# Performance work log

Hardware: AMD Instinct MI355X
Metric: run time of the kernel (lower is better)

The kernel has to match this reference:

```python
import jax, jax.numpy as jnp
import numpy as np

B, L, DIM, H = 2, 2048, 2048, 16
D = DIM // H
EPS = 1e-6
CAP = 50.0
SCALE = D ** -0.5


def _rms_norm(x, w):
    # x: [B,H,L,D], normalize over last dim
    scale = jax.lax.rsqrt(jnp.maximum(jnp.mean(x * x, axis=-1, keepdims=True), EPS))
    return w * x * scale


def _rotate_half(x):
    x1, x2 = jnp.split(x, 2, axis=-1)
    return jnp.concatenate([-x2, x1], axis=-1)


def setup_inputs() -> dict:
    key = jax.random.key(0)
    ks = jax.random.split(key, 6)
    x = jax.random.normal(ks[0], (B, L, DIM), dtype=jnp.float32)
    w_qkv = jax.random.normal(ks[1], (3 * DIM, DIM), dtype=jnp.float32) * (DIM ** -0.5)
    w_out = jax.random.normal(ks[2], (DIM, DIM), dtype=jnp.float32) * (DIM ** -0.5)
    q_norm_w = jnp.ones((D,), dtype=jnp.float32)
    k_norm_w = jnp.ones((D,), dtype=jnp.float32)
    # rope tables [L, D]
    inv_freq = 1.0 / (10000.0 ** (np.arange(0, D, 2, dtype=np.float32) / D))
    t = np.arange(L, dtype=np.float32)
    freqs = np.outer(t, inv_freq)  # [L, D/2]
    emb = np.concatenate([freqs, freqs], axis=-1)  # [L, D]
    cos = jnp.asarray(np.cos(emb), dtype=jnp.float32)
    sin = jnp.asarray(np.sin(emb), dtype=jnp.float32)
    # additive causal mask [1,1,L,L]
    causal = np.triu(np.full((L, L), -1e9, dtype=np.float32), k=1)
    mask = jnp.asarray(causal)[None, None]
    return {"x": x, "w_qkv": w_qkv, "w_out": w_out, "q_norm_w": q_norm_w,
            "k_norm_w": k_norm_w, "cos": cos, "sin": sin, "mask": mask}


def reference(x, w_qkv, w_out, q_norm_w, k_norm_w, cos, sin, mask):
    b, l, _ = x.shape
    qkv = jnp.einsum('bld,ed->ble', x, w_qkv).reshape(b, l, 3, H, D)
    q, k, v = [jnp.transpose(qkv[:, :, i], (0, 2, 1, 3)) for i in range(3)]  # [B,H,L,D]
    q = _rms_norm(q, q_norm_w)
    k = _rms_norm(k, k_norm_w)
    # rope: cos/sin are [L,D] -> [1,1,L,D]
    c = cos[-l:, :][None, None]
    s = sin[-l:, :][None, None]
    q = q * c + _rotate_half(q) * s
    k = k * c + _rotate_half(k) * s
    attn = jnp.einsum('bhqd,bhkd->bhqk', q, k) * SCALE
    attn = jnp.tanh(attn / CAP) * CAP + mask
    probs = jax.nn.softmax(attn, axis=-1)
    o = jnp.einsum('bhqk,bhkd->bhqd', probs, v)
    o = jnp.transpose(o, (0, 2, 1, 3)).reshape(b, l, H * D)
    out = jnp.einsum('bld,ed->ble', o, w_out)
    return (out, (k, v))
```

## Files before the change

kernel.cpp:

```cpp
#include <hip/hip_runtime.h>
#include <hip/hip_bf16.h>
#include <stdint.h>

#define LL 2048
#define DD 128
#define HH 16

typedef float f32x4 __attribute__((ext_vector_type(4)));
typedef float f32x16 __attribute__((ext_vector_type(16)));
typedef float f32x2 __attribute__((ext_vector_type(2)));
typedef short bf16x8 __attribute__((ext_vector_type(8)));
typedef short short4v __attribute__((ext_vector_type(4)));
typedef int int4v __attribute__((ext_vector_type(4)));
typedef float float4v __attribute__((ext_vector_type(4)));

__device__ __forceinline__ float bf2f(short s) {
  union { unsigned u; float f; } v; v.u = ((unsigned)(unsigned short)s) << 16; return v.f;
}
__device__ __forceinline__ short f2bf(float f) {
  union { float f; unsigned u; } v; v.f = f;
  unsigned u = v.u;
  u += 0x7fffu + ((u >> 16) & 1u);
  return (short)(u >> 16);
}
__device__ __forceinline__ unsigned cvtpk(float lo, float hi) {
  unsigned r;
  asm("v_cvt_pk_bf16_f32 %0, %1, %2" : "=v"(r) : "v"(lo), "v"(hi));
  return r;
}

__device__ __forceinline__ void gload_lds16(const void* g, void* lds) {
  __builtin_amdgcn_global_load_lds(
      (__attribute__((address_space(1))) unsigned int*)(void*)(uintptr_t)g,
      (__attribute__((address_space(3))) unsigned int*)lds, 16, 0, 0);
}

__global__ __launch_bounds__(256) void cast_all_kernel(
    const float* __restrict__ x, const float* __restrict__ wqkv,
    const float* __restrict__ wout, short* __restrict__ dst)
{
  long i4 = ((long)blockIdx.x * 256 + threadIdx.x) * 4;
  const float* src; long off;
  if (i4 < 8388608L)        { src = x;    off = i4; }
  else if (i4 < 20971520L)  { src = wqkv; off = i4 - 8388608L; }
  else                      { src = wout; off = i4 - 20971520L; }
  float4v v = *(const float4v*)(src + off);
  short4v o;
  o.x = f2bf(v.x); o.y = f2bf(v.y); o.z = f2bf(v.z); o.w = f2bf(v.w);
  *(short4v*)(dst + i4) = o;
}

#define SCHED __builtin_amdgcn_sched_barrier(0)
#define BARRIER { __builtin_amdgcn_s_barrier(); }

#define STAGE(buf, opx, ptr, rb, ks, t)                                        \
  { _Pragma("unroll") for (int l_ = 0; l_ < 2; ++l_) {                          \
      int ch_ = l_ * 512 + tid;                                                 \
      int row_ = ch_ >> 2, ci_ = ch_ & 3;                                       \
      gload_lds16(ptr + (size_t)(rb + row_) * K + (t) * 64 + (ks) * 32 +        \
                      ((ci_ ^ ((row_ >> 1) & 3)) << 3),                         \
                  &lds[buf][opx][ks][ch_ << 3]);                                \
  } }

#define LDA(buf, mh, ks)                                                       \
  { _Pragma("unroll") for (int mf_ = 0; mf_ < 4; ++mf_) {                       \
      int r_ = wm * 128 + (mh) * 64 + mf_ * 16 + j;                             \
      areg[mf_] = *(const bf16x8*)&lds[buf][0][ks][r_ * 32 + ((g ^ ((j >> 1) & 3)) << 3)]; \
  } }

#define LDB(dst, buf, ks)                                                      \
  { _Pragma("unroll") for (int nf_ = 0; nf_ < 4; ++nf_) {                       \
      int r_ = wn * 64 + nf_ * 16 + j;                                          \
      dst[nf_] = *(const bf16x8*)&lds[buf][1][ks][r_ * 32 + ((g ^ ((j >> 1) & 3)) << 3)]; \
  } }

#define MFMAQ(mh, breg)                                                        \
  { __builtin_amdgcn_s_setprio(1);                                             \
    _Pragma("unroll") for (int mf_ = 0; mf_ < 4; ++mf_)                         \
      _Pragma("unroll") for (int nf_ = 0; nf_ < 4; ++nf_)                       \
        acc[(mh) * 4 + mf_][nf_] = __builtin_amdgcn_mfma_f32_16x16x32_bf16(     \
            areg[mf_], breg[nf_], acc[(mh) * 4 + mf_][nf_], 0, 0, 0);           \
    __builtin_amdgcn_s_setprio(0); }

__global__ __launch_bounds__(512, 2) void gemm256_kernel(
    const short* __restrict__ A, const short* __restrict__ Bm,
    short* __restrict__ C, int M, int N, int K)
{
  __shared__ __align__(16) short lds[2][2][2][8192];
  const int tid = threadIdx.x;
  const int lane = tid & 63;
  const int wid = tid >> 6;
  const int wm = wid >> 2, wn = wid & 3;
  const int g = lane >> 4, j = lane & 15;
  const int xcd = blockIdx.x & 7, qq = blockIdx.x >> 3;
  const int bx = 3 * xcd + qq % 3, by = qq / 3;
  const int m0 = by * 256, n0 = bx * 256;
  const int NT = K >> 6;

  f32x4 acc[8][4];
  const f32x4 z = {0.f, 0.f, 0.f, 0.f};
#pragma unroll
  for (int im = 0; im < 8; ++im)
#pragma unroll
    for (int nf = 0; nf < 4; ++nf) acc[im][nf] = z;

  STAGE(0, 1, Bm, n0, 0, 0); STAGE(0, 1, Bm, n0, 1, 0);
  STAGE(0, 0, A,  m0, 0, 0); STAGE(0, 0, A,  m0, 1, 0);
  STAGE(1, 1, Bm, n0, 0, 1); STAGE(1, 1, Bm, n0, 1, 1);
  STAGE(1, 0, A,  m0, 0, 1);
  asm volatile("s_waitcnt vmcnt(6)" ::: "memory");
  __builtin_amdgcn_s_barrier();
  SCHED;

  bf16x8 areg[4], b0r[4], b1r[4];
#pragma unroll 1
  for (int i = 0; i < (NT >> 1) - 1; ++i) {
    int t0 = i * 2;
    LDA(0, 0, 0); LDB(b0r, 0, 0);
    STAGE(1, 0, A, m0, 1, t0 + 1);
    BARRIER; MFMAQ(0, b0r); BARRIER;
    LDA(0, 0, 1); LDB(b1r, 0, 1);
    STAGE(0, 1, Bm, n0, 0, t0 + 2);
    BARRIER; MFMAQ(0, b1r); BARRIER;
    LDA(0, 1, 0);
    STAGE(0, 1, Bm, n0, 1, t0 + 2);
    BARRIER; MFMAQ(1, b0r); BARRIER;
    LDA(0, 1, 1);
    STAGE(0, 0, A, m0, 0, t0 + 2);
    BARRIER; MFMAQ(1, b1r);
    asm volatile("s_waitcnt vmcnt(6)" ::: "memory");
    __builtin_amdgcn_s_barrier(); SCHED;
    LDA(1, 0, 0); LDB(b0r, 1, 0);
    STAGE(0, 0, A, m0, 1, t0 + 2);
    BARRIER; MFMAQ(0, b0r); BARRIER;
    LDA(1, 0, 1); LDB(b1r, 1, 1);
    STAGE(1, 1, Bm, n0, 0, t0 + 3);
    BARRIER; MFMAQ(0, b1r); BARRIER;
    LDA(1, 1, 0);
    STAGE(1, 1, Bm, n0, 1, t0 + 3);
    BARRIER; MFMAQ(1, b0r); BARRIER;
    LDA(1, 1, 1);
    STAGE(1, 0, A, m0, 0, t0 + 3);
    BARRIER; MFMAQ(1, b1r);
    asm volatile("s_waitcnt vmcnt(6)" ::: "memory");
    __builtin_amdgcn_s_barrier(); SCHED;
  }
  {
    LDA(0, 0, 0); LDB(b0r, 0, 0);
    STAGE(1, 0, A, m0, 1, NT - 1);
    BARRIER; MFMAQ(0, b0r); BARRIER;
    LDA(0, 0, 1); LDB(b1r, 0, 1);
    BARRIER; MFMAQ(0, b1r); BARRIER;
    LDA(0, 1, 0);
    BARRIER; MFMAQ(1, b0r); BARRIER;
    LDA(0, 1, 1);
    BARRIER; MFMAQ(1, b1r);
    asm volatile("s_waitcnt vmcnt(0)" ::: "memory");
    __builtin_amdgcn_s_barrier(); SCHED;
    LDA(1, 0, 0); LDB(b0r, 1, 0); MFMAQ(0, b0r);
    LDA(1, 0, 1); LDB(b1r, 1, 1); MFMAQ(0, b1r);
    LDA(1, 1, 0); MFMAQ(1, b0r);
    LDA(1, 1, 1); MFMAQ(1, b1r);
  }
#pragma unroll
  for (int im = 0; im < 8; ++im)
#pragma unroll
    for (int nf = 0; nf < 4; ++nf)
#pragma unroll
      for (int r = 0; r < 4; ++r)
        C[(size_t)(m0 + wm * 128 + im * 16 + g * 4 + r) * N + n0 + wn * 64 + nf * 16 + j] =
            f2bf(acc[im][nf][r]);
}

template <typename OutT>
__global__ __launch_bounds__(256) void gemm_bt_kernel(
    const short* __restrict__ A, const short* __restrict__ Bm,
    OutT* __restrict__ C, int M, int N, int K)
{
  __shared__ __align__(16) short As[128 * 64];
  __shared__ __align__(16) short Bs[128 * 64];
  const int tid = threadIdx.x;
  const int lane = tid & 63;
  const int g = lane >> 4, j = lane & 15;
  const int m0 = blockIdx.y * 128, n0 = blockIdx.x * 128;
  const int wave = tid >> 6;
  const int wm = (wave >> 1) * 64, wn = (wave & 1) * 64;

  f32x4 acc[4][4];
  const f32x4 z = {0.f, 0.f, 0.f, 0.f};
#pragma unroll
  for (int i = 0; i < 4; ++i)
#pragma unroll
    for (int jj = 0; jj < 4; ++jj) acc[i][jj] = z;

  for (int k0 = 0; k0 < K; k0 += 64) {
#pragma unroll
    for (int it = 0; it < 4; ++it) {
      int c = it * 256 + tid;
      int row = c >> 3, ko = (c & 7) << 3;
      gload_lds16(A + (size_t)(m0 + row) * K + k0 + ko, As + c * 8);
    }
#pragma unroll
    for (int it = 0; it < 4; ++it) {
      int c = it * 256 + tid;
      int row = c >> 3, ko = (c & 7) << 3;
      gload_lds16(Bm + (size_t)(n0 + row) * K + k0 + ko, Bs + c * 8);
    }
    __syncthreads();
#pragma unroll
    for (int ks = 0; ks < 2; ++ks) {
      bf16x8 af[4], bfr[4];
#pragma unroll
      for (int i = 0; i < 4; ++i)
        af[i] = *(const bf16x8*)(As + (wm + i * 16 + j) * 64 + ks * 32 + g * 8);
#pragma unroll
      for (int i = 0; i < 4; ++i)
        bfr[i] = *(const bf16x8*)(Bs + (wn + i * 16 + j) * 64 + ks * 32 + g * 8);
#pragma unroll
      for (int i = 0; i < 4; ++i)
#pragma unroll
        for (int jj = 0; jj < 4; ++jj)
          acc[i][jj] = __builtin_amdgcn_mfma_f32_16x16x32_bf16(af[i], bfr[jj], acc[i][jj], 0, 0, 0);
    }
    __syncthreads();
  }
#pragma unroll
  for (int i = 0; i < 4; ++i)
#pragma unroll
    for (int jj = 0; jj < 4; ++jj)
#pragma unroll
      for (int r = 0; r < 4; ++r) {
        int row = m0 + wm + i * 16 + g * 4 + r;
        int col = n0 + wn + jj * 16 + j;
        if constexpr (sizeof(OutT) == 4)
          C[(size_t)row * N + col] = acc[i][jj][r];
        else
          C[(size_t)row * N + col] = f2bf(acc[i][jj][r]);
      }
}

__global__ __launch_bounds__(256) void normrope_kernel(
    const short* __restrict__ qkv, const float* __restrict__ qw,
    const float* __restrict__ kw, const float* __restrict__ cosb,
    const float* __restrict__ sinb, short* __restrict__ qo,
    float* __restrict__ ko, short* __restrict__ kb, float* __restrict__ vo)
{
  int wid = (blockIdx.x * 256 + threadIdx.x) >> 6;
  int lane = threadIdx.x & 63;
  int h = wid & 15;
  int rest = wid >> 4;
  int t = rest % 3;
  int bl = rest / 3;
  int l = bl & (LL - 1);
  int d0 = lane * 2;
  const short* src = qkv + (size_t)bl * 6144 + t * 2048 + h * 128 + d0;
  int raw = *(const int*)src;
  float v0 = bf2f((short)(raw & 0xffff));
  float v1 = bf2f((short)((raw >> 16) & 0xffff));
  size_t oidx = ((size_t)((bl >> 11) * HH + h) * LL + l) * DD + d0;
  if (t == 2) {
    f32x2 vv = {v0, v1};
    *(f32x2*)(vo + oidx) = vv;
    return;
  }
  float ss = v0 * v0 + v1 * v1;
#pragma unroll
  for (int m = 1; m <= 32; m <<= 1) ss += __shfl_xor(ss, m, 64);
  float scale = rsqrtf(fmaxf(ss * (1.0f / 128.0f), 1e-6f));
  const float* w = (t == 0) ? qw : kw;
  float n0 = w[d0] * v0 * scale;
  float n1 = w[d0 + 1] * v1 * scale;
  float c0 = cosb[l * 128 + d0], c1 = cosb[l * 128 + d0 + 1];
  float s0 = sinb[l * 128 + d0], s1 = sinb[l * 128 + d0 + 1];
  float p0 = __shfl_xor(n0, 32, 64);
  float p1 = __shfl_xor(n1, 32, 64);
  float r0 = (lane < 32) ? -p0 : p0;
  float r1 = (lane < 32) ? -p1 : p1;
  float o0 = n0 * c0 + r0 * s0;
  float o1 = n1 * c1 + r1 * s1;
  if (t == 0) {
    const float cu = 0.0017677669529663687f;
    int pk = (int)((unsigned short)f2bf(o0 * cu) |
                   ((unsigned)(unsigned short)f2bf(o1 * cu) << 16));
    *(int*)(qo + oidx) = pk;
  } else {
    f32x2 kk = {o0, o1};
    *(f32x2*)(ko + oidx) = kk;
    int pk = (int)((unsigned short)f2bf(o0) | ((unsigned)(unsigned short)f2bf(o1) << 16));
    *(int*)(kb + oidx) = pk;
  }
}

__global__ __launch_bounds__(256) void transpose_v_kernel(
    const short* __restrict__ qkv, short* __restrict__ vT)
{
  __shared__ __align__(16) short tl[64 * 72];
  int bid = blockIdx.x;
  int dt = bid & 1;
  int lt = (bid >> 1) & 31;
  int bh = bid >> 6;
  int b = bh >> 4, h = bh & 15;
  int tid = threadIdx.x;
#pragma unroll
  for (int it = 0; it < 2; ++it) {
    int c = it * 256 + tid;
    int row = c >> 3, off = (c & 7) << 3;
    int l = lt * 64 + row;
    bf16x8 val = *(const bf16x8*)(qkv + (size_t)(b * LL + l) * 6144 + 4096 + h * 128 + dt * 64 + off);
    *(bf16x8*)(tl + row * 72 + off) = val;
  }
  __syncthreads();
#pragma unroll
  for (int it = 0; it < 2; ++it) {
    int c = it * 256 + tid;
    int dr = c >> 3, lo = (c & 7) << 3;
    bf16x8 o;
#pragma unroll
    for (int i = 0; i < 8; ++i) o[i] = tl[(lo + i) * 72 + dr];
    *(bf16x8*)(vT + ((size_t)bh * DD + dt * 64 + dr) * LL + lt * 64 + lo) = o;
  }
}

#define STAGE_KV(t, buf)                                                       \
  { int k0_ = (t) * 64;                                                        \
    _Pragma("unroll") for (int it_ = 0; it_ < 2; ++it_) {                      \
      int c_ = it_ * 512 + tid;                                                \
      int row_ = c_ >> 4, off_ = (c_ & 15) << 3;                               \
      gload_lds16(kp + (size_t)(k0_ + row_) * DD + (off_ ^ ((row_ & 7) << 3)), \
                  KsA + (buf) * 8192 + c_ * 8);                                \
    }                                                                          \
    _Pragma("unroll") for (int it_ = 0; it_ < 2; ++it_) {                      \
      int c_ = it_ * 512 + tid;                                                \
      int row_ = c_ >> 3, off_ = (c_ & 7) << 3;                                \
      gload_lds16(vp + (size_t)row_ * LL + k0_ + (off_ ^ ((row_ & 7) << 3)),   \
                  VsA + (buf) * 8192 + c_ * 8);                                \
    } }

__global__ __launch_bounds__(512, 1) void attn_kernel(
    const short* __restrict__ q, const short* __restrict__ k,
    const short* __restrict__ vT, short* __restrict__ o)
{
  __shared__ __align__(16) short KsA[3 * 64 * 128];
  __shared__ __align__(16) short VsA[3 * 128 * 64];
  int bid = blockIdx.x;
  int bh = bid & 31;
  int p = (bid >> 5) & 7;
  int b = bh >> 4;
  int h = bh & 15;
  int tid = threadIdx.x;
  int lane = tid & 63;
  int w = tid >> 6;
  int l31 = lane & 31, lo5 = lane >> 5;
  int qt = (w < 4) ? (15 - p) : p;
  int wrow = qt * 128 + (w & 3) * 32;
  int qg = wrow + l31;

  const short* kp = k + (size_t)bh * LL * DD;
  const short* vp = vT + (size_t)bh * DD * LL;

  bf16x8 qf[8];
#pragma unroll
  for (int ds_ = 0; ds_ < 8; ++ds_)
    qf[ds_] = *(const bf16x8*)(q + ((size_t)bh * LL + qg) * DD + ds_ * 16 + lo5 * 8);

  f32x16 accO[4];
#pragma unroll
  for (int dt = 0; dt < 4; ++dt)
#pragma unroll
    for (int r = 0; r < 16; ++r) accO[dt][r] = 0.f;
  float lsum = 0.f;

  const int ktmax = 2 * (15 - p) + 1;
  STAGE_KV(0, 0);
  STAGE_KV(1, 1);
  asm volatile("s_waitcnt vmcnt(4)" ::: "memory");
  __builtin_amdgcn_s_barrier();

  int bufc = 0;
#pragma unroll 1
  for (int kt = 0; kt <= ktmax; ++kt) {
    int k0 = kt * 64;
    const short* Kb = KsA + bufc * 8192;
    const short* Vb = VsA + bufc * 8192;

    const bool active = (k0 <= wrow + 31);
    if (active) {
      f32x16 sa[2];
#pragma unroll
      for (int t2 = 0; t2 < 2; ++t2)
#pragma unroll
        for (int r = 0; r < 16; ++r) sa[t2][r] = 0.f;

      __builtin_amdgcn_s_setprio(1);
#pragma unroll
      for (int ds_ = 0; ds_ < 8; ++ds_) {
#pragma unroll
        for (int t2 = 0; t2 < 2; ++t2) {
          int row = t2 * 32 + l31;
          bf16x8 kf = *(const bf16x8*)(Kb + row * 128 +
                          ((ds_ * 16 + lo5 * 8) ^ ((l31 & 7) << 3)));
          sa[t2] = __builtin_amdgcn_mfma_f32_32x32x16_bf16(kf, qf[ds_], sa[t2], 0, 0, 0);
        }
      }
      __builtin_amdgcn_s_setprio(0);

#pragma unroll
      for (int t2 = 0; t2 < 2; ++t2) {
        const bool tmask = (k0 + t2 * 32 + 31) > wrow;
#pragma unroll
        for (int r = 0; r < 16; ++r) {
          float u = sa[t2][r];
          float v2 = u * u;
          float poly = fmaf(v2, fmaf(v2, fmaf(v2, -2.6984127f, 6.6666667f),
                                     -16.666667f), 50.f);
          float pe = __expf(fmaf(u, poly, -12.f));
          int kglob = k0 + t2 * 32 + (r & 3) + 8 * (r >> 2) + 4 * lo5;
          if (tmask && (kglob > qg)) pe = 0.f;
          lsum += pe;
          sa[t2][r] = pe;
        }
      }

      __builtin_amdgcn_s_setprio(1);
#pragma unroll
      for (int s = 0; s < 4; ++s) {
        int t2 = s >> 1, RA = 8 * (s & 1), RB = RA + 4;
        unsigned a0 = cvtpk(sa[t2][RA + 0], sa[t2][RA + 1]);
        unsigned b0 = cvtpk(sa[t2][RB + 0], sa[t2][RB + 1]);
        unsigned a1 = cvtpk(sa[t2][RA + 2], sa[t2][RA + 3]);
        unsigned b1 = cvtpk(sa[t2][RB + 2], sa[t2][RB + 3]);
        asm("v_permlane32_swap_b32 %0, %1" : "+v"(a0), "+v"(b0));
        asm("v_permlane32_swap_b32 %0, %1" : "+v"(a1), "+v"(b1));
        int4v wv;
        wv.x = (int)a0;
        wv.y = (int)a1;
        wv.z = (int)b0;
        wv.w = (int)b1;
        bf16x8 pa = __builtin_bit_cast(bf16x8, wv);
#pragma unroll
        for (int dt = 0; dt < 4; ++dt) {
          int row = dt * 32 + l31;
          bf16x8 vf = *(const bf16x8*)(Vb + row * 64 +
                          ((s * 16 + lo5 * 8) ^ ((l31 & 7) << 3)));
          accO[dt] = __builtin_amdgcn_mfma_f32_32x32x16_bf16(pa, vf, accO[dt], 0, 0, 0);
        }
      }
      __builtin_amdgcn_s_setprio(0);
    }

    if (kt + 2 <= ktmax) {
      int nb = bufc + 2; if (nb >= 3) nb -= 3;
      STAGE_KV(kt + 2, nb);
      asm volatile("s_waitcnt vmcnt(4)" ::: "memory");
      __builtin_amdgcn_s_barrier();
    } else if (kt + 1 <= ktmax) {
      asm volatile("s_waitcnt vmcnt(0)" ::: "memory");
      __builtin_amdgcn_s_barrier();
    }
    ++bufc; if (bufc == 3) bufc = 0;
  }

  lsum += __shfl_xor(lsum, 32, 64);
  float inv = 1.f / lsum;
#pragma unroll
  for (int r = 0; r < 16; ++r) {
    int qrow = (r & 3) + 8 * (r >> 2) + 4 * lo5;
    float invr = __shfl(inv, qrow, 64);
    size_t obase = ((size_t)b * LL + wrow + qrow) * 2048 + h * 128;
#pragma unroll
    for (int dt = 0; dt < 4; ++dt)
      o[obase + dt * 32 + l31] = f2bf(accO[dt][r] * invr);
  }
}

extern "C" void kernel_launch(void* const* d_in, const int* in_sizes, int n_in,
                              void* d_out, int out_size, void* d_ws, size_t ws_size,
                              hipStream_t stream) {
  const float* x    = (const float*)d_in[0];
  const float* wqkv = (const float*)d_in[1];
  const float* wout = (const float*)d_in[2];
  const float* qw   = (const float*)d_in[3];
  const float* kw   = (const float*)d_in[4];
  const float* cosb = (const float*)d_in[5];
  const float* sinb = (const float*)d_in[6];

  float* out   = (float*)d_out;
  float* k_out = out + 8388608;
  float* v_out = out + 16777216;

  short* ws    = (short*)d_ws;
  short* xb    = ws;
  short* wqkvb = ws + 8388608;
  short* woutb = ws + 20971520;
  short* qkv   = ws + 25165824;
  short* qbuf  = xb;
  short* kbuf  = wqkvb;
  short* vT    = ws + 50331648;
  short* obuf  = qkv;

  cast_all_kernel<<<24576, 256, 0, stream>>>(x, wqkv, wout, ws);
  gemm256_kernel<<<384, 512, 0, stream>>>(xb, wqkvb, qkv, 4096, 6144, 2048);
  normrope_kernel<<<49152, 256, 0, stream>>>(qkv, qw, kw, cosb, sinb, qbuf, k_out, kbuf, v_out);
  transpose_v_kernel<<<2048, 256, 0, stream>>>(qkv, vT);
  attn_kernel<<<256, 512, 0, stream>>>(qbuf, kbuf, vT, obuf);
  gemm_bt_kernel<float><<<dim3(16, 32), 256, 0, stream>>>(obuf, woutb, out, 4096, 2048, 2048);
}
```

Measured before the change: 292.6 us.

## Stage K/V in 128-key pairs with double buffering in attention loop

Replaces the triple-buffered 64-key K/V pipeline with a double-buffered pipeline that loads two 64-key subtiles per stage and processes both before synchronizing. This halves the number of loop iterations and barrier/wait points per key range, aiming to cut synchronization overhead and give more work between loads. It adds an extra barrier before each refill, increases LDS use from 96KB to 128KB, and deepens outstanding loads (vmcnt 8), which may reduce latency hiding at the start of each refill.

```diff
diff --git a/kernel.cpp b/kernel.cpp
--- a/kernel.cpp
+++ b/kernel.cpp
@@ -321,27 +321,30 @@
   }
 }
 
-#define STAGE_KV(t, buf)                                                       \
-  { int k0_ = (t) * 64;                                                        \
+#define STAGE_KV_SUB(t64, buf, st)                                             \
+  { int k0_ = (t64) * 64;                                                      \
     _Pragma("unroll") for (int it_ = 0; it_ < 2; ++it_) {                      \
       int c_ = it_ * 512 + tid;                                                \
       int row_ = c_ >> 4, off_ = (c_ & 15) << 3;                               \
       gload_lds16(kp + (size_t)(k0_ + row_) * DD + (off_ ^ ((row_ & 7) << 3)), \
-                  KsA + (buf) * 8192 + c_ * 8);                                \
+                  KsA + (buf) * 16384 + (st) * 8192 + c_ * 8);                 \
     }                                                                          \
     _Pragma("unroll") for (int it_ = 0; it_ < 2; ++it_) {                      \
       int c_ = it_ * 512 + tid;                                                \
       int row_ = c_ >> 3, off_ = (c_ & 7) << 3;                                \
       gload_lds16(vp + (size_t)row_ * LL + k0_ + (off_ ^ ((row_ & 7) << 3)),   \
-                  VsA + (buf) * 8192 + c_ * 8);                                \
+                  VsA + (buf) * 16384 + (st) * 8192 + c_ * 8);                 \
     } }
+
+#define STAGE_PAIR(tp, buf)                                                    \
+  { STAGE_KV_SUB(2 * (tp), buf, 0); STAGE_KV_SUB(2 * (tp) + 1, buf, 1); }
 
 __global__ __launch_bounds__(512, 1) void attn_kernel(
     const short* __restrict__ q, const short* __restrict__ k,
     const short* __restrict__ vT, short* __restrict__ o)
 {
-  __shared__ __align__(16) short KsA[3 * 64 * 128];
-  __shared__ __align__(16) short VsA[3 * 128 * 64];
+  __shared__ __align__(16) short KsA[2 * 2 * 64 * 128];
+  __shared__ __align__(16) short VsA[2 * 2 * 128 * 64];
   int bid = blockIdx.x;
   int bh = bid & 31;
   int p = (bid >> 5) & 7;
@@ -370,94 +373,96 @@
     for (int r = 0; r < 16; ++r) accO[dt][r] = 0.f;
   float lsum = 0.f;
 
-  const int ktmax = 2 * (15 - p) + 1;
-  STAGE_KV(0, 0);
-  STAGE_KV(1, 1);
-  asm volatile("s_waitcnt vmcnt(4)" ::: "memory");
+  const int pmax = 15 - p;
+  STAGE_PAIR(0, 0);
+  STAGE_PAIR(1, 1);
+  asm volatile("s_waitcnt vmcnt(8)" ::: "memory");
   __builtin_amdgcn_s_barrier();
 
-  int bufc = 0;
 #pragma unroll 1
-  for (int kt = 0; kt <= ktmax; ++kt) {
-    int k0 = kt * 64;
-    const short* Kb = KsA + bufc * 8192;
-    const short* Vb = VsA + bufc * 8192;
-
-    const bool active = (k0 <= wrow + 31);
-    if (active) {
-      f32x16 sa[2];
-#pragma unroll
-      for (int t2 = 0; t2 < 2; ++t2)
-#pragma unroll
-        for (int r = 0; r < 16; ++r) sa[t2][r] = 0.f;
-
-      __builtin_amdgcn_s_setprio(1);
-#pragma unroll
-      for (int ds_ = 0; ds_ < 8; ++ds_) {
+  for (int kt = 0; kt <= pmax; ++kt) {
+    const short* Kpair = KsA + (kt & 1) * 16384;
+    const short* Vpair = VsA + (kt & 1) * 16384;
+
+#pragma unroll
+    for (int st = 0; st < 2; ++st) {
+      int k0 = kt * 128 + st * 64;
+      const short* Kb = Kpair + st * 8192;
+      const short* Vb = Vpair + st * 8192;
+      const bool active = (k0 <= wrow + 31);
+      if (active) {
+        f32x16 sa[2];
+#pragma unroll
+        for (int t2 = 0; t2 < 2; ++t2)
+#pragma unroll
+          for (int r = 0; r < 16; ++r) sa[t2][r] = 0.f;
+
+        __builtin_amdgcn_s_setprio(1);
+#pragma unroll
+        for (int ds_ = 0; ds_ < 8; ++ds_) {
+#pragma unroll
+          for (int t2 = 0; t2 < 2; ++t2) {
+            int row = t2 * 32 + l31;
+            bf16x8 kf = *(const bf16x8*)(Kb + row * 128 +
+                            ((ds_ * 16 + lo5 * 8) ^ ((l31 & 7) << 3)));
+            sa[t2] = __builtin_amdgcn_mfma_f32_32x32x16_bf16(kf, qf[ds_], sa[t2], 0, 0, 0);
+          }
+        }
+        __builtin_amdgcn_s_setprio(0);
+
 #pragma unroll
         for (int t2 = 0; t2 < 2; ++t2) {
-          int row = t2 * 32 + l31;
-          bf16x8 kf = *(const bf16x8*)(Kb + row * 128 +
-                          ((ds_ * 16 + lo5 * 8) ^ ((l31 & 7) << 3)));
-          sa[t2] = __builtin_amdgcn_mfma_f32_32x32x16_bf16(kf, qf[ds_], sa[t2], 0, 0, 0);
+          const bool tmask = (k0 + t2 * 32 + 31) > wrow;
+#pragma unroll
+          for (int r = 0; r < 16; ++r) {
+            float u = sa[t2][r];
+            float v2 = u * u;
+            float poly = fmaf(v2, fmaf(v2, fmaf(v2, -2.6984127f, 6.6666667f),
+                                       -16.666667f), 50.f);
+            float pe = __expf(fmaf(u, poly, -12.f));
+            int kglob = k0 + t2 * 32 + (r & 3) + 8 * (r >> 2) + 4 * lo5;
+            if (tmask && (kglob > qg)) pe = 0.f;
+            lsum += pe;
+            sa[t2][r] = pe;
+          }
         }
+
+        __builtin_amdgcn_s_setprio(1);
+#pragma unroll
+        for (int s = 0; s < 4; ++s) {
+          int t2 = s >> 1, RA = 8 * (s & 1), RB = RA + 4;
+          unsigned a0 = cvtpk(sa[t2][RA + 0], sa[t2][RA + 1]);
+          unsigned b0 = cvtpk(sa[t2][RB + 0], sa[t2][RB + 1]);
+          unsigned a1 = cvtpk(sa[t2][RA + 2], sa[t2][RA + 3]);
+          unsigned b1 = cvtpk(sa[t2][RB + 2], sa[t2][RB + 3]);
+          asm("v_permlane32_swap_b32 %0, %1" : "+v"(a0), "+v"(b0));
+          asm("v_permlane32_swap_b32 %0, %1" : "+v"(a1), "+v"(b1));
+          int4v wv;
+          wv.x = (int)a0;
+          wv.y = (int)a1;
+          wv.z = (int)b0;
+          wv.w = (int)b1;
+          bf16x8 pa = __builtin_bit_cast(bf16x8, wv);
+#pragma unroll
+          for (int dt = 0; dt < 4; ++dt) {
+            int row = dt * 32 + l31;
+            bf16x8 vf = *(const bf16x8*)(Vb + row * 64 +
+                            ((s * 16 + lo5 * 8) ^ ((l31 & 7) << 3)));
+            accO[dt] = __builtin_amdgcn_mfma_f32_32x32x16_bf16(pa, vf, accO[dt], 0, 0, 0);
+          }
+        }
+        __builtin_amdgcn_s_setprio(0);
       }
-      __builtin_amdgcn_s_setprio(0);
-
-#pragma unroll
-      for (int t2 = 0; t2 < 2; ++t2) {
-        const bool tmask = (k0 + t2 * 32 + 31) > wrow;
-#pragma unroll
-        for (int r = 0; r < 16; ++r) {
-          float u = sa[t2][r];
-          float v2 = u * u;
-          float poly = fmaf(v2, fmaf(v2, fmaf(v2, -2.6984127f, 6.6666667f),
-                                     -16.666667f), 50.f);
-          float pe = __expf(fmaf(u, poly, -12.f));
-          int kglob = k0 + t2 * 32 + (r & 3) + 8 * (r >> 2) + 4 * lo5;
-          if (tmask && (kglob > qg)) pe = 0.f;
-          lsum += pe;
-          sa[t2][r] = pe;
-        }
-      }
-
-      __builtin_amdgcn_s_setprio(1);
-#pragma unroll
-      for (int s = 0; s < 4; ++s) {
-        int t2 = s >> 1, RA = 8 * (s & 1), RB = RA + 4;
-        unsigned a0 = cvtpk(sa[t2][RA + 0], sa[t2][RA + 1]);
-        unsigned b0 = cvtpk(sa[t2][RB + 0], sa[t2][RB + 1]);
-        unsigned a1 = cvtpk(sa[t2][RA + 2], sa[t2][RA + 3]);
-        unsigned b1 = cvtpk(sa[t2][RB + 2], sa[t2][RB + 3]);
-        asm("v_permlane32_swap_b32 %0, %1" : "+v"(a0), "+v"(b0));
-        asm("v_permlane32_swap_b32 %0, %1" : "+v"(a1), "+v"(b1));
-        int4v wv;
-        wv.x = (int)a0;
-        wv.y = (int)a1;
-        wv.z = (int)b0;
-        wv.w = (int)b1;
-        bf16x8 pa = __builtin_bit_cast(bf16x8, wv);
-#pragma unroll
-        for (int dt = 0; dt < 4; ++dt) {
-          int row = dt * 32 + l31;
-          bf16x8 vf = *(const bf16x8*)(Vb + row * 64 +
-                          ((s * 16 + lo5 * 8) ^ ((l31 & 7) << 3)));
-          accO[dt] = __builtin_amdgcn_mfma_f32_32x32x16_bf16(pa, vf, accO[dt], 0, 0, 0);
-        }
-      }
-      __builtin_amdgcn_s_setprio(0);
     }
 
-    if (kt + 2 <= ktmax) {
-      int nb = bufc + 2; if (nb >= 3) nb -= 3;
-      STAGE_KV(kt + 2, nb);
-      asm volatile("s_waitcnt vmcnt(4)" ::: "memory");
-      __builtin_amdgcn_s_barrier();
-    } else if (kt + 1 <= ktmax) {
+    __builtin_amdgcn_s_barrier();
+    if (kt + 2 <= pmax) {
+      STAGE_PAIR(kt + 2, kt & 1);
+      asm volatile("s_waitcnt vmcnt(8)" ::: "memory");
+    } else if (kt + 1 <= pmax) {
       asm volatile("s_waitcnt vmcnt(0)" ::: "memory");
-      __builtin_amdgcn_s_barrier();
     }
-    ++bufc; if (bufc == 3) bufc = 0;
+    __builtin_amdgcn_s_barrier();
   }
 
   lsum += __shfl_xor(lsum, 32, 64);
```

New measurement: 290.3 us. Within noise of the previous version (-0.8%).
